# Performance work log

Measured on AMD Instinct MI355X. Metric: run time of the kernel, lower is better.

The kernel has to match this reference:

```python
import jax, jax.numpy as jnp
import numpy as np

NUM_NODES = 200000
NUM_EDGES = 640000
RANK = 16
EMBED_DIM = 128


def setup_inputs() -> dict:
    key = jax.random.key(0)
    k1, k2, k3 = jax.random.split(key, 3)
    U = jax.random.normal(k1, (NUM_NODES, RANK), dtype=jnp.float32)
    V = jax.random.normal(k2, (RANK, EMBED_DIM), dtype=jnp.float32)
    edge_index = jax.random.randint(k3, (2, NUM_EDGES), 0, NUM_NODES, dtype=jnp.int64)
    return {"U": U, "V": V, "edge_index": edge_index}


def reference(U, V, edge_index):
    # Low-rank projection: [N, r] @ [r, d] -> [N, d]
    embeddings = jnp.matmul(U, V)
    src, dst = edge_index[0], edge_index[1]
    # Mean aggregation (PyG MessagePassing aggr='mean', source_to_target):
    # gather messages from source nodes, segment-mean into destination nodes.
    msgs = embeddings[src]  # [E, d]
    summed = jax.ops.segment_sum(msgs, dst, num_segments=NUM_NODES)  # [N, d]
    counts = jax.ops.segment_sum(jnp.ones((edge_index.shape[1],), dtype=embeddings.dtype),
                                 dst, num_segments=NUM_NODES)  # [N]
    denom = jnp.maximum(counts, 1.0)  # isolated nodes -> 0 output (scatter-mean semantics)
    return summed / denom[:, None]
```

## Files before the change

kernel.cpp:

```cpp
#include <hip/hip_runtime.h>

#define RANK 16
#define EMBED_DIM 128
#define CAP 16

typedef float floatx4 __attribute__((ext_vector_type(4)));

__global__ __launch_bounds__(256) void fill_slots(
        const int* __restrict__ eiw,
        int* __restrict__ cnt,
        int* __restrict__ ovfcnt,
        int* __restrict__ slots,
        int* __restrict__ ovf,
        int E, int nwords) {
    __shared__ int iflag;
    if (threadIdx.x == 0) iflag = 0;
    __syncthreads();
    {
        int w = 2 * threadIdx.x + 1;
        unsigned int v = (w < nwords) ? ((const unsigned int*)eiw)[w] : 0u;
        if (v) atomicOr(&iflag, 1);
    }
    __syncthreads();
    const bool is32 = (iflag != 0);

    const int base = (blockIdx.x * 256 + threadIdx.x) * 4;
    if (base >= E) return;

    int srcs[4], dsts[4];
    int ne;
    if ((E & 3) == 0 && base + 3 < E) {
        ne = 4;
        if (is32) {
            int4 s = *(const int4*)(eiw + base);
            int4 d = *(const int4*)(eiw + E + base);
            srcs[0] = s.x; srcs[1] = s.y; srcs[2] = s.z; srcs[3] = s.w;
            dsts[0] = d.x; dsts[1] = d.y; dsts[2] = d.z; dsts[3] = d.w;
        } else {
            const int4* p = (const int4*)(eiw + 2 * base);
            const int4* q = (const int4*)(eiw + 2 * (E + base));
            int4 v0 = p[0], v1 = p[1], d0 = q[0], d1 = q[1];
            srcs[0] = v0.x; srcs[1] = v0.z; srcs[2] = v1.x; srcs[3] = v1.z;
            dsts[0] = d0.x; dsts[1] = d0.z; dsts[2] = d1.x; dsts[3] = d1.z;
        }
    } else {
        ne = 0;
        for (int e = base; e < E && e < base + 4; ++e, ++ne) {
            srcs[ne] = is32 ? eiw[e] : eiw[2 * e];
            dsts[ne] = is32 ? eiw[E + e] : eiw[2 * (E + e)];
        }
    }

#pragma unroll
    for (int j = 0; j < 4; ++j) {
        if (j >= ne) break;
        int dst = dsts[j];
        int pos = atomicAdd(&cnt[dst], 1);
        if (pos < CAP) {
            slots[(size_t)dst * CAP + pos] = srcs[j];
        } else {
            int o = atomicAdd(ovfcnt, 1);
            ovf[2 * o]     = srcs[j];
            ovf[2 * o + 1] = dst;
        }
    }
}

__global__ __launch_bounds__(256) void gather_project(
        const float* __restrict__ U,
        const float* __restrict__ V,
        const int* __restrict__ cnt,
        const int* __restrict__ slots,
        const int* __restrict__ ovfcnt,
        const int* __restrict__ ovf,
        float* __restrict__ out, int N) {
    __shared__ float4 Vs4[RANK * EMBED_DIM / 4];
    __shared__ float accs[32][RANK];
    __shared__ float sinv[32];
    __shared__ int   scnt[32];
    __shared__ int4  sslot4[32 * CAP / 4];

    const int t = threadIdx.x;
    const float4* V4 = (const float4*)V;
    Vs4[t]       = V4[t];
    Vs4[t + 256] = V4[t + 256];

    const int n0 = blockIdx.x * 32;

    if (t < 32) {
        int n = n0 + t;
        int c = (n < N) ? cnt[n] : 0;
        scnt[t] = c;
        sinv[t] = 1.0f / fmaxf((float)c, 1.0f);
    }
    if (t < 128) {
        const int4* g4 = (const int4*)(slots + (size_t)n0 * CAP);
        if (n0 + (t >> 2) < N) sslot4[t] = g4[t];
    }
    __syncthreads();

    const int* sslot = (const int*)sslot4;
    const int g = t >> 4;
    const int j = t & 15;
#pragma unroll
    for (int half = 0; half < 2; ++half) {
        int nd = half * 16 + g;
        int n = n0 + nd;
        float acc = 0.f;
        if (n < N) {
            int deg = scnt[nd];
            int k = deg < CAP ? deg : CAP;
            for (int e = 0; e < k; ++e) {
                int s = sslot[nd * CAP + e];
                acc += U[(size_t)s * RANK + j];
            }
            if (deg > CAP) {
                int m = *ovfcnt;
                for (int i = 0; i < m; ++i)
                    if (ovf[2 * i + 1] == n)
                        acc += U[(size_t)ovf[2 * i] * RANK + j];
            }
        }
        accs[nd][j] = acc;
    }
    __syncthreads();

    const int q = t & 31;
    const int w = t >> 5;
#pragma unroll
    for (int r = 0; r < 4; ++r) {
        int nd = 4 * w + r;
        float4 a4 = make_float4(0.f, 0.f, 0.f, 0.f);
#pragma unroll
        for (int k = 0; k < RANK; ++k) {
            float a = accs[nd][k];
            float4 v = Vs4[k * 32 + q];
            a4.x = fmaf(a, v.x, a4.x);
            a4.y = fmaf(a, v.y, a4.y);
            a4.z = fmaf(a, v.z, a4.z);
            a4.w = fmaf(a, v.w, a4.w);
        }
        float s = sinv[nd];
        int n = n0 + nd;
        if (n < N) {
            floatx4 o;
            o.x = a4.x * s; o.y = a4.y * s; o.z = a4.z * s; o.w = a4.w * s;
            __builtin_nontemporal_store(
                o, (floatx4*)out + (size_t)n * (EMBED_DIM / 4) + q);
        }
    }
}

extern "C" void kernel_launch(void* const* d_in, const int* in_sizes, int n_in,
                              void* d_out, int out_size, void* d_ws, size_t ws_size,
                              hipStream_t stream) {
    const float* U = (const float*)d_in[0];
    const float* V = (const float*)d_in[1];
    const int* EI = (const int*)d_in[2];
    float* out = (float*)d_out;

    const int N = in_sizes[0] / RANK;
    const int E = in_sizes[2] / 2;
    const int nwords = in_sizes[2];

    int* wsI = (int*)d_ws;
    int* cnt = wsI;
    int* ovfcnt = wsI + N;
    const int slots_off = (N + 1 + 15) & ~15;
    int* slots = wsI + slots_off;
    int* ovf = slots + (size_t)N * CAP;

    hipMemsetAsync(d_ws, 0, (size_t)(N + 1) * sizeof(int), stream);

    fill_slots<<<(E + 1023) / 1024, 256, 0, stream>>>(
        EI, cnt, ovfcnt, slots, ovf, E, nwords);

    gather_project<<<(N + 31) / 32, 256, 0, stream>>>(
        U, V, cnt, slots, ovfcnt, ovf, out, N);
}
```

Baseline: 187.7 us.

## Persistent gather blocks, unrolled slot gather, and finer edge parallelism in fill

fill_slots now handles 2 edges per thread instead of 4, launching twice as many threads to expose more atomic parallelism. gather_project becomes a grid-stride persistent kernel capped at 2560 blocks, so V is loaded into shared memory once per block rather than once per 32-node tile. The per-node gather loop is unrolled by 4 so several independent U loads are in flight at once. The costs are extra per-tile syncs and fewer resident blocks to hide latency.

```diff
diff --git a/kernel.cpp b/kernel.cpp
--- a/kernel.cpp
+++ b/kernel.cpp
@@ -24,35 +24,34 @@
     __syncthreads();
     const bool is32 = (iflag != 0);
 
-    const int base = (blockIdx.x * 256 + threadIdx.x) * 4;
+    const int base = (blockIdx.x * 256 + threadIdx.x) * 2;
     if (base >= E) return;
 
-    int srcs[4], dsts[4];
+    int srcs[2], dsts[2];
     int ne;
-    if ((E & 3) == 0 && base + 3 < E) {
-        ne = 4;
+    if ((E & 1) == 0 && base + 1 < E) {
+        ne = 2;
         if (is32) {
-            int4 s = *(const int4*)(eiw + base);
-            int4 d = *(const int4*)(eiw + E + base);
-            srcs[0] = s.x; srcs[1] = s.y; srcs[2] = s.z; srcs[3] = s.w;
-            dsts[0] = d.x; dsts[1] = d.y; dsts[2] = d.z; dsts[3] = d.w;
+            int2 s = *(const int2*)(eiw + base);
+            int2 d = *(const int2*)(eiw + E + base);
+            srcs[0] = s.x; srcs[1] = s.y;
+            dsts[0] = d.x; dsts[1] = d.y;
         } else {
-            const int4* p = (const int4*)(eiw + 2 * base);
-            const int4* q = (const int4*)(eiw + 2 * (E + base));
-            int4 v0 = p[0], v1 = p[1], d0 = q[0], d1 = q[1];
-            srcs[0] = v0.x; srcs[1] = v0.z; srcs[2] = v1.x; srcs[3] = v1.z;
-            dsts[0] = d0.x; dsts[1] = d0.z; dsts[2] = d1.x; dsts[3] = d1.z;
+            int4 sv = *(const int4*)(eiw + 2 * base);
+            int4 dv = *(const int4*)(eiw + 2 * (E + base));
+            srcs[0] = sv.x; srcs[1] = sv.z;
+            dsts[0] = dv.x; dsts[1] = dv.z;
         }
     } else {
         ne = 0;
-        for (int e = base; e < E && e < base + 4; ++e, ++ne) {
+        for (int e = base; e < E && e < base + 2; ++e, ++ne) {
             srcs[ne] = is32 ? eiw[e] : eiw[2 * e];
             dsts[ne] = is32 ? eiw[E + e] : eiw[2 * (E + e)];
         }
     }
 
 #pragma unroll
-    for (int j = 0; j < 4; ++j) {
+    for (int j = 0; j < 2; ++j) {
         if (j >= ne) break;
         int dst = dsts[j];
         int pos = atomicAdd(&cnt[dst], 1);
@@ -73,7 +72,7 @@
         const int* __restrict__ slots,
         const int* __restrict__ ovfcnt,
         const int* __restrict__ ovf,
-        float* __restrict__ out, int N) {
+        float* __restrict__ out, int N, int ntiles) {
     __shared__ float4 Vs4[RANK * EMBED_DIM / 4];
     __shared__ float accs[32][RANK];
     __shared__ float sinv[32];
@@ -85,68 +84,83 @@
     Vs4[t]       = V4[t];
     Vs4[t + 256] = V4[t + 256];
 
-    const int n0 = blockIdx.x * 32;
-
-    if (t < 32) {
-        int n = n0 + t;
-        int c = (n < N) ? cnt[n] : 0;
-        scnt[t] = c;
-        sinv[t] = 1.0f / fmaxf((float)c, 1.0f);
-    }
-    if (t < 128) {
-        const int4* g4 = (const int4*)(slots + (size_t)n0 * CAP);
-        if (n0 + (t >> 2) < N) sslot4[t] = g4[t];
-    }
-    __syncthreads();
-
-    const int* sslot = (const int*)sslot4;
     const int g = t >> 4;
     const int j = t & 15;
-#pragma unroll
-    for (int half = 0; half < 2; ++half) {
-        int nd = half * 16 + g;
-        int n = n0 + nd;
-        float acc = 0.f;
-        if (n < N) {
-            int deg = scnt[nd];
-            int k = deg < CAP ? deg : CAP;
-            for (int e = 0; e < k; ++e) {
-                int s = sslot[nd * CAP + e];
-                acc += U[(size_t)s * RANK + j];
-            }
-            if (deg > CAP) {
-                int m = *ovfcnt;
-                for (int i = 0; i < m; ++i)
-                    if (ovf[2 * i + 1] == n)
-                        acc += U[(size_t)ovf[2 * i] * RANK + j];
-            }
-        }
-        accs[nd][j] = acc;
-    }
-    __syncthreads();
-
     const int q = t & 31;
     const int w = t >> 5;
+    const int* sslot = (const int*)sslot4;
+
+    for (int tile = blockIdx.x; tile < ntiles; tile += gridDim.x) {
+        const int n0 = tile * 32;
+        __syncthreads();
+
+        if (t < 32) {
+            int n = n0 + t;
+            int c = (n < N) ? cnt[n] : 0;
+            scnt[t] = c;
+            sinv[t] = 1.0f / fmaxf((float)c, 1.0f);
+        }
+        if (t < 128) {
+            const int4* g4 = (const int4*)(slots + (size_t)n0 * CAP);
+            if (n0 + (t >> 2) < N) sslot4[t] = g4[t];
+        }
+        __syncthreads();
+
 #pragma unroll
-    for (int r = 0; r < 4; ++r) {
-        int nd = 4 * w + r;
-        float4 a4 = make_float4(0.f, 0.f, 0.f, 0.f);
+        for (int half = 0; half < 2; ++half) {
+            int nd = half * 16 + g;
+            int n = n0 + nd;
+            float acc = 0.f;
+            if (n < N) {
+                int deg = scnt[nd];
+                int k = deg < CAP ? deg : CAP;
+                const int* sl = sslot + nd * CAP;
+                for (int e = 0; e < k; e += 4) {
+                    int s0 = sl[e];
+                    int s1 = (e + 1 < k) ? sl[e + 1] : s0;
+                    int s2 = (e + 2 < k) ? sl[e + 2] : s0;
+                    int s3 = (e + 3 < k) ? sl[e + 3] : s0;
+                    float u0 = U[(size_t)s0 * RANK + j];
+                    float u1 = U[(size_t)s1 * RANK + j];
+                    float u2 = U[(size_t)s2 * RANK + j];
+                    float u3 = U[(size_t)s3 * RANK + j];
+                    acc += u0;
+                    acc += (e + 1 < k) ? u1 : 0.f;
+                    acc += (e + 2 < k) ? u2 : 0.f;
+                    acc += (e + 3 < k) ? u3 : 0.f;
+                }
+                if (deg > CAP) {
+                    int m = *ovfcnt;
+                    for (int i = 0; i < m; ++i)
+                        if (ovf[2 * i + 1] == n)
+                            acc += U[(size_t)ovf[2 * i] * RANK + j];
+                }
+            }
+            accs[nd][j] = acc;
+        }
+        __syncthreads();
+
 #pragma unroll
-        for (int k = 0; k < RANK; ++k) {
-            float a = accs[nd][k];
-            float4 v = Vs4[k * 32 + q];
-            a4.x = fmaf(a, v.x, a4.x);
-            a4.y = fmaf(a, v.y, a4.y);
-            a4.z = fmaf(a, v.z, a4.z);
-            a4.w = fmaf(a, v.w, a4.w);
-        }
-        float s = sinv[nd];
-        int n = n0 + nd;
-        if (n < N) {
-            floatx4 o;
-            o.x = a4.x * s; o.y = a4.y * s; o.z = a4.z * s; o.w = a4.w * s;
-            __builtin_nontemporal_store(
-                o, (floatx4*)out + (size_t)n * (EMBED_DIM / 4) + q);
+        for (int r = 0; r < 4; ++r) {
+            int nd = 4 * w + r;
+            float4 a4 = make_float4(0.f, 0.f, 0.f, 0.f);
+#pragma unroll
+            for (int k = 0; k < RANK; ++k) {
+                float a = accs[nd][k];
+                float4 v = Vs4[k * 32 + q];
+                a4.x = fmaf(a, v.x, a4.x);
+                a4.y = fmaf(a, v.y, a4.y);
+                a4.z = fmaf(a, v.z, a4.z);
+                a4.w = fmaf(a, v.w, a4.w);
+            }
+            float s = sinv[nd];
+            int n = n0 + nd;
+            if (n < N) {
+                floatx4 o;
+                o.x = a4.x * s; o.y = a4.y * s; o.z = a4.z * s; o.w = a4.w * s;
+                __builtin_nontemporal_store(
+                    o, (floatx4*)out + (size_t)n * (EMBED_DIM / 4) + q);
+            }
         }
     }
 }
@@ -170,11 +184,13 @@
     int* slots = wsI + slots_off;
     int* ovf = slots + (size_t)N * CAP;
 
-    hipMemsetAsync(d_ws, 0, (size_t)(N + 1) * sizeof(int), stream);
+    (void)hipMemsetAsync(d_ws, 0, (size_t)(N + 1) * sizeof(int), stream);
 
-    fill_slots<<<(E + 1023) / 1024, 256, 0, stream>>>(
+    fill_slots<<<(E / 2 + 255) / 256, 256, 0, stream>>>(
         EI, cnt, ovfcnt, slots, ovf, E, nwords);
 
-    gather_project<<<(N + 31) / 32, 256, 0, stream>>>(
-        U, V, cnt, slots, ovfcnt, ovf, out, N);
+    const int ntiles = (N + 31) / 32;
+    const int nblk = ntiles < 2560 ? ntiles : 2560;
+    gather_project<<<nblk, 256, 0, stream>>>(
+        U, V, cnt, slots, ovfcnt, ovf, out, N, ntiles);
 }
```

New measurement: 180.4 us. -3.9%, faster.
